# Optimization experiments

Hardware: AMD Instinct MI355X
Metric: run time of the kernel (lower is better)

Reference implementation:

```python
import jax, jax.numpy as jnp
import numpy as np
from math import factorial, sqrt

# ---- e3nn-style real Wigner-3j (Clebsch-Gordan) construction ----
L1, L2, LOUT, LMID = 3, 3, 3, 4

def _cg_coef(j1, m1, j2, m2, j3, m3):
    if m1 + m2 != m3:
        return 0.0
    f = factorial
    vmin = max(0, j2 - j3 - m1, j1 - j3 + m2)
    vmax = min(j1 + j2 - j3, j1 - m1, j2 + m2)
    pref = sqrt((2 * j3 + 1) * f(j3 + j1 - j2) * f(j3 - j1 + j2) * f(j1 + j2 - j3) / f(j1 + j2 + j3 + 1))
    pref *= sqrt(f(j3 + m3) * f(j3 - m3) * f(j1 + m1) * f(j1 - m1) * f(j2 + m2) * f(j2 - m2))
    s = 0.0
    for v in range(vmin, vmax + 1):
        s += (-1) ** v / (f(v) * f(j1 + j2 - j3 - v) * f(j1 - m1 - v) * f(j2 + m2 - v)
                          * f(j3 - j2 + m1 + v) * f(j3 - j1 - m2 + v))
    return pref * s

def _su2_cg(l1, l2, l3):
    C = np.zeros((2 * l1 + 1, 2 * l2 + 1, 2 * l3 + 1))
    for m1 in range(-l1, l1 + 1):
        for m2 in range(-l2, l2 + 1):
            m3 = m1 + m2
            if -l3 <= m3 <= l3:
                C[l1 + m1, l2 + m2, l3 + m3] = _cg_coef(l1, m1, l2, m2, l3, m3)
    return C

def _q(l):  # real->complex SH change of basis (e3nn convention)
    q = np.zeros((2 * l + 1, 2 * l + 1), dtype=np.complex128)
    for m in range(-l, 0):
        q[l + m, l + abs(m)] = 1 / np.sqrt(2)
        q[l + m, l - abs(m)] = -1j / np.sqrt(2)
    q[l, l] = 1.0
    for m in range(1, l + 1):
        q[l + m, l + abs(m)] = (-1) ** m / np.sqrt(2)
        q[l + m, l - abs(m)] = 1j * (-1) ** m / np.sqrt(2)
    return (-1j) ** l * q

def _w3j(l1, l2, l3):
    C = _su2_cg(l1, l2, l3).astype(np.complex128)
    C = np.einsum('ij,kl,mn,ikn->jlm', _q(l1), _q(l2), np.conj(_q(l3).T), C)
    C = np.real(C)
    return (C / np.linalg.norm(C)).astype(np.float32)

def _instructions(lmax1, lmax2, lmax_out):
    ins = [(a, b, c)
           for a in range(lmax1 + 1) for b in range(lmax2 + 1) for c in range(lmax_out + 1)
           if abs(a - b) <= c <= a + b and (a + b + c) % 2 == 0]
    cnt = {}
    for _, _, c in ins:
        cnt[c] = cnt.get(c, 0) + 1
    # normalization='component', path_normalization='element' with all mul=1
    pw = np.array([sqrt((2 * c + 1) / cnt[c]) for _, _, c in ins], dtype=np.float32)
    return ins, pw

INS1, PW1 = _instructions(L1, L2, LMID)      # 27 paths
INS21, PW21 = _instructions(L1, LMID, LOUT)  # 27 paths
INS22, PW22 = _instructions(L2, LMID, LOUT)  # 27 paths
W3J = {k: jnp.asarray(_w3j(*k)) for k in set(INS1) | set(INS21) | set(INS22)}

def _tp(x, y, w, ins, pw, lmax_out):
    # FullyConnectedTensorProduct with multiplicity-1 SH irreps.
    # x: [E, (l1+1)^2], y: [E, (l2+1)^2] -> [E, (lmax_out+1)^2]
    out = jnp.zeros((x.shape[0], (lmax_out + 1) ** 2), dtype=x.dtype)
    for i, (a, b, c) in enumerate(ins):
        xa = x[:, a * a:(a + 1) ** 2]
        yb = y[:, b * b:(b + 1) ** 2]
        z = jnp.einsum('ijk,ei,ej->ek', W3J[(a, b, c)], xa, yb)
        out = out.at[:, c * c:(c + 1) ** 2].add((pw[i] * w[i]) * z)
    return out

E, C = 200000, 16
B = (LOUT + 1) ** 2  # 16

def setup_inputs() -> dict:
    k = jax.random.split(jax.random.key(0), 5)
    return {
        'x': jax.random.normal(k[0], (E, B, C), jnp.float32),
        'y': jax.random.normal(k[1], (E, B, C), jnp.float32),
        'w1': jax.random.normal(k[2], (len(INS1),), jnp.float32),
        'w21': jax.random.normal(k[3], (len(INS21),), jnp.float32),
        'w22': jax.random.normal(k[4], (len(INS22),), jnp.float32),
    }

def reference(x, y, w1, w21, w22):
    xm = x.mean(2)  # [E, 16]
    ym = y.mean(2)  # [E, 16]
    mid = _tp(xm, ym, w1, INS1, PW1, LMID)  # [E, 25]
    out = (x + y
           + _tp(xm, mid, w21, INS21, PW21, LOUT)[..., None]
           + _tp(ym, mid, w22, INS22, PW22, LOUT)[..., None])
    return out
```

## Files before the change

### kernel.cpp

```cpp
#include <hip/hip_runtime.h>


struct W3JT { double v[9][9][9]; };

constexpr double dfact(int n) { double r = 1.0; for (int i = 2; i <= n; ++i) r *= (double)i; return r; }

constexpr double csqrt(double x) {
  if (x <= 0.0) return 0.0;
  double g = x > 1.0 ? x : 1.0;
  for (int i = 0; i < 80; ++i) g = 0.5 * (g + x / g);
  return g;
}

constexpr double cg_coef(int j1, int m1, int j2, int m2, int j3, int m3) {
  if (m1 + m2 != m3) return 0.0;
  int vmin = 0;
  if (j2 - j3 - m1 > vmin) vmin = j2 - j3 - m1;
  if (j1 - j3 + m2 > vmin) vmin = j1 - j3 + m2;
  int vmax = j1 + j2 - j3;
  if (j1 - m1 < vmax) vmax = j1 - m1;
  if (j2 + m2 < vmax) vmax = j2 + m2;
  double pref = csqrt((2.0 * j3 + 1.0) * dfact(j3 + j1 - j2) * dfact(j3 - j1 + j2) * dfact(j1 + j2 - j3) / dfact(j1 + j2 + j3 + 1));
  pref *= csqrt(dfact(j3 + m3) * dfact(j3 - m3) * dfact(j1 + m1) * dfact(j1 - m1) * dfact(j2 + m2) * dfact(j2 - m2));
  double s = 0.0;
  for (int v = vmin; v <= vmax; ++v) {
    double t = 1.0 / (dfact(v) * dfact(j1 + j2 - j3 - v) * dfact(j1 - m1 - v) * dfact(j2 + m2 - v) * dfact(j3 - j2 + m1 + v) * dfact(j3 - j1 - m2 + v));
    s += (v & 1) ? -t : t;
  }
  return pref * s;
}

struct QCol { int n; int row[2]; double re[2]; double im[2]; };

constexpr QCol qcol(int l, int col) {
  QCol q{};
  const int lm = l & 3;
  const double pr = (lm == 0) ? 1.0 : (lm == 2) ? -1.0 : 0.0;
  const double pi = (lm == 1) ? -1.0 : (lm == 3) ? 1.0 : 0.0;
  const int mu = col - l;
  const int am = mu < 0 ? -mu : mu;
  const double is2 = 0.70710678118654752440;
  if (mu == 0) {
    q.n = 1; q.row[0] = l;
    q.re[0] = pr; q.im[0] = pi;
  } else {
    const double s = (am & 1) ? -1.0 : 1.0;
    double a0 = 0.0, b0 = 0.0, a1 = 0.0, b1 = 0.0;
    if (mu > 0) { a0 = is2; b0 = 0.0;  a1 = s * is2; b1 = 0.0; }
    else        { a0 = 0.0; b0 = -is2; a1 = 0.0;     b1 = s * is2; }
    q.n = 2;
    q.row[0] = l - am; q.row[1] = l + am;
    q.re[0] = a0 * pr - b0 * pi; q.im[0] = a0 * pi + b0 * pr;
    q.re[1] = a1 * pr - b1 * pi; q.im[1] = a1 * pi + b1 * pr;
  }
  return q;
}

constexpr W3JT make_w3j(int l1, int l2, int l3) {
  W3JT R{};
  double C[9][9][9]{};
  for (int m1 = -l1; m1 <= l1; ++m1)
    for (int m2 = -l2; m2 <= l2; ++m2) {
      int m3 = m1 + m2;
      if (m3 >= -l3 && m3 <= l3)
        C[l1 + m1][l2 + m2][l3 + m3] = cg_coef(l1, m1, l2, m2, l3, m3);
    }
  double nrm = 0.0;
  for (int j = 0; j < 2 * l1 + 1; ++j) {
    QCol q1 = qcol(l1, j);
    for (int l = 0; l < 2 * l2 + 1; ++l) {
      QCol q2 = qcol(l2, l);
      for (int m = 0; m < 2 * l3 + 1; ++m) {
        QCol q3 = qcol(l3, m);
        double re = 0.0;
        for (int a = 0; a < q1.n; ++a)
          for (int b = 0; b < q2.n; ++b)
            for (int c = 0; c < q3.n; ++c) {
              double cv = C[q1.row[a]][q2.row[b]][q3.row[c]];
              if (cv == 0.0) continue;
              double ar = q1.re[a], ai = q1.im[a];
              double br = q2.re[b], bi = q2.im[b];
              double cr = q3.re[c], ci = -q3.im[c];
              double abr = ar * br - ai * bi;
              double abi = ar * bi + ai * br;
              double prr = abr * cr - abi * ci;
              re += prr * cv;
            }
        R.v[j][l][m] = re;
        nrm += re * re;
      }
    }
  }
  double n = csqrt(nrm);
  if (n > 0.0)
    for (int j = 0; j < 2 * l1 + 1; ++j)
      for (int l = 0; l < 2 * l2 + 1; ++l)
        for (int m = 0; m < 2 * l3 + 1; ++m)
          R.v[j][l][m] /= n;
  return R;
}

constexpr int CNT1[5] = {4, 6, 7, 6, 4};
constexpr int CNT2[4] = {4, 7, 8, 8};

#define NZCHK(V) ((V) > 1e-12 || (V) < -1e-12)

#define TP_MID(IDX, A, B, C) do { \
  constexpr W3JT T = make_w3j(A, B, C); \
  constexpr double PW = csqrt((2.0 * (C) + 1.0) / (double)CNT1[(C)]); \
  const float wi = w1p[IDX]; \
  float u[2 * (A) + 1]; \
  _Pragma("unroll") for (int i = 0; i < 2 * (A) + 1; ++i) u[i] = wi * xm[(A) * (A) + i]; \
  _Pragma("unroll") for (int i = 0; i < 2 * (A) + 1; ++i) { \
    _Pragma("unroll") for (int j = 0; j < 2 * (B) + 1; ++j) { \
      const float p_ = u[i] * ym[(B) * (B) + j]; \
      _Pragma("unroll") for (int k = 0; k < 2 * (C) + 1; ++k) { \
        if (NZCHK(T.v[i][j][k])) \
          mid[(C) * (C) + k] = __builtin_fmaf((float)(T.v[i][j][k] * PW), p_, mid[(C) * (C) + k]); \
      } \
    } \
  } \
} while (0)

#define TP_OUT(IDX, A, B, C) do { \
  constexpr W3JT T = make_w3j(A, B, C); \
  constexpr double PW = csqrt((2.0 * (C) + 1.0) / (double)CNT2[(C)]); \
  const float wa = w21p[IDX]; \
  const float wb = w22p[IDX]; \
  float u[2 * (A) + 1]; \
  _Pragma("unroll") for (int i = 0; i < 2 * (A) + 1; ++i) \
    u[i] = wa * xm[(A) * (A) + i] + wb * ym[(A) * (A) + i]; \
  _Pragma("unroll") for (int i = 0; i < 2 * (A) + 1; ++i) { \
    _Pragma("unroll") for (int j = 0; j < 2 * (B) + 1; ++j) { \
      const float p_ = u[i] * mid[(B) * (B) + j]; \
      _Pragma("unroll") for (int k = 0; k < 2 * (C) + 1; ++k) { \
        if (NZCHK(T.v[i][j][k])) \
          tv[(C) * (C) + k] = __builtin_fmaf((float)(T.v[i][j][k] * PW), p_, tv[(C) * (C) + k]); \
      } \
    } \
  } \
} while (0)

__global__ __launch_bounds__(512) void cg2_v15(
    const float4* __restrict__ x4, const float4* __restrict__ y4,
    const float* __restrict__ w1p, const float* __restrict__ w21p,
    const float* __restrict__ w22p, float4* __restrict__ o4, int E)
{
  __shared__ float lmx[128 * 32];
  __shared__ float ltv[128 * 16];

  const int eL = threadIdx.x >> 2;
  const int g  = threadIdx.x & 3;
  const int e  = blockIdx.x * 128 + eL;
  const bool ok = (e < E);
  const int base = e * 64 + g;

  float4 s[16];
  float px[16], py[16];
  if (ok) {
#pragma unroll
    for (int k = 0; k < 16; ++k) {
      const float4 xv = x4[base + 4 * k];
      const float4 yv = y4[base + 4 * k];
      s[k].x = xv.x + yv.x; s[k].y = xv.y + yv.y;
      s[k].z = xv.z + yv.z; s[k].w = xv.w + yv.w;
      px[k] = (xv.x + xv.y) + (xv.z + xv.w);
      py[k] = (yv.x + yv.y) + (yv.z + yv.w);
    }
  } else {
#pragma unroll
    for (int k = 0; k < 16; ++k) { px[k] = 0.f; py[k] = 0.f; }
  }

#pragma unroll
  for (int k = 0; k < 16; ++k) {
    float rx = px[k] + __shfl_xor(px[k], 1);
    rx += __shfl_xor(rx, 2);
    float ry = py[k] + __shfl_xor(py[k], 1);
    ry += __shfl_xor(ry, 2);
    px[k] = rx * (1.0f / 16.0f);
    py[k] = ry * (1.0f / 16.0f);
  }

  if (ok) {
#pragma unroll
    for (int u = 0; u < 4; ++u) {
      const int j = 4 * g + u;
      lmx[eL * 32 + ((j + eL) & 31)]      = px[j];
      lmx[eL * 32 + ((16 + j + eL) & 31)] = py[j];
    }
  }
  __syncthreads();

  if (threadIdx.x < 128) {
    const int q = threadIdx.x;
    const bool ok2 = (blockIdx.x * 128 + q < E);
    float xm[16], ym[16];
#pragma unroll
    for (int j = 0; j < 16; ++j) xm[j] = lmx[q * 32 + ((j + q) & 31)];
#pragma unroll
    for (int j = 0; j < 16; ++j) ym[j] = lmx[q * 32 + ((16 + j + q) & 31)];

    float mid[25];
#pragma unroll
    for (int k = 0; k < 25; ++k) mid[k] = 0.f;

    TP_MID( 0, 0, 0, 0);
    TP_MID( 1, 0, 1, 1);
    TP_MID( 2, 0, 2, 2);
    TP_MID( 3, 0, 3, 3);
    TP_MID( 4, 1, 0, 1);
    TP_MID( 5, 1, 1, 0);
    TP_MID( 6, 1, 1, 2);
    TP_MID( 7, 1, 2, 1);
    TP_MID( 8, 1, 2, 3);
    TP_MID( 9, 1, 3, 2);
    TP_MID(10, 1, 3, 4);
    TP_MID(11, 2, 0, 2);
    TP_MID(12, 2, 1, 1);
    TP_MID(13, 2, 1, 3);
    TP_MID(14, 2, 2, 0);
    TP_MID(15, 2, 2, 2);
    TP_MID(16, 2, 2, 4);
    TP_MID(17, 2, 3, 1);
    TP_MID(18, 2, 3, 3);
    TP_MID(19, 3, 0, 3);
    TP_MID(20, 3, 1, 2);
    TP_MID(21, 3, 1, 4);
    TP_MID(22, 3, 2, 1);
    TP_MID(23, 3, 2, 3);
    TP_MID(24, 3, 3, 0);
    TP_MID(25, 3, 3, 2);
    TP_MID(26, 3, 3, 4);

    float tv[16];
#pragma unroll
    for (int k = 0; k < 16; ++k) tv[k] = 0.f;

    TP_OUT( 0, 0, 0, 0);
    TP_OUT( 1, 0, 1, 1);
    TP_OUT( 2, 0, 2, 2);
    TP_OUT( 3, 0, 3, 3);
    TP_OUT( 4, 1, 0, 1);
    TP_OUT( 5, 1, 1, 0);
    TP_OUT( 6, 1, 1, 2);
    TP_OUT( 7, 1, 2, 1);
    TP_OUT( 8, 1, 2, 3);
    TP_OUT( 9, 1, 3, 2);
    TP_OUT(10, 1, 4, 3);
    TP_OUT(11, 2, 0, 2);
    TP_OUT(12, 2, 1, 1);
    TP_OUT(13, 2, 1, 3);
    TP_OUT(14, 2, 2, 0);
    TP_OUT(15, 2, 2, 2);
    TP_OUT(16, 2, 3, 1);
    TP_OUT(17, 2, 3, 3);
    TP_OUT(18, 2, 4, 2);
    TP_OUT(19, 3, 0, 3);
    TP_OUT(20, 3, 1, 2);
    TP_OUT(21, 3, 2, 1);
    TP_OUT(22, 3, 2, 3);
    TP_OUT(23, 3, 3, 0);
    TP_OUT(24, 3, 3, 2);
    TP_OUT(25, 3, 4, 1);
    TP_OUT(26, 3, 4, 3);

    if (ok2) {
#pragma unroll
      for (int k = 0; k < 16; ++k) ltv[q * 16 + ((k + q) & 15)] = tv[k];
    }
  }
  __syncthreads();

  if (ok) {
#pragma unroll
    for (int k = 0; k < 16; ++k) {
      const float t = ltv[eL * 16 + ((k + eL) & 15)];
      float4 o;
      o.x = s[k].x + t;
      o.y = s[k].y + t;
      o.z = s[k].z + t;
      o.w = s[k].w + t;
      o4[base + 4 * k] = o;
    }
  }
}

extern "C" void kernel_launch(void* const* d_in, const int* in_sizes, int n_in,
                              void* d_out, int out_size, void* d_ws, size_t ws_size,
                              hipStream_t stream) {
  const float4* x4 = (const float4*)d_in[0];
  const float4* y4 = (const float4*)d_in[1];
  const float* w1p = (const float*)d_in[2];
  const float* w21p = (const float*)d_in[3];
  const float* w22p = (const float*)d_in[4];
  float4* o4 = (float4*)d_out;

  const int E = in_sizes[0] / 256;
  const int block = 512;
  const int grid = (E + 127) / 128;

  cg2_v15<<<grid, block, 0, stream>>>(x4, y4, w1p, w21p, w22p, o4, E);
}
```

Baseline: 145.2 us.

## Process two edges per thread, store residual as bf16, group paths by output

Halves the block to 256 threads, with each thread loading two edges' x and y. The x+y residual is kept in registers as packed bf16 to cut register pressure. The tensor-product stages accumulate per output degree and read means and mid values from shared memory instead of holding large register arrays. The aim is to reduce register use and raise occupancy and memory parallelism, at the cost of bf16 rounding error in the residual term.

New measurement: 203.9 us. 1.4x slower.

```diff
diff --git a/kernel.cpp b/kernel.cpp
--- a/kernel.cpp
+++ b/kernel.cpp
@@ -105,183 +105,181 @@
 
 #define NZCHK(V) ((V) > 1e-12 || (V) < -1e-12)
 
-#define TP_MID(IDX, A, B, C) do { \
+#define LXM(J) lmx[q * 32 + (((J) + q) & 31)]
+#define LYM(J) lmx[q * 32 + ((16 + (J) + q) & 31)]
+
+#define TPM(IDX, A, B, C, ACC) do { \
   constexpr W3JT T = make_w3j(A, B, C); \
   constexpr double PW = csqrt((2.0 * (C) + 1.0) / (double)CNT1[(C)]); \
   const float wi = w1p[IDX]; \
-  float u[2 * (A) + 1]; \
-  _Pragma("unroll") for (int i = 0; i < 2 * (A) + 1; ++i) u[i] = wi * xm[(A) * (A) + i]; \
+  float u_[2 * (A) + 1], yv_[2 * (B) + 1]; \
+  _Pragma("unroll") for (int i = 0; i < 2 * (A) + 1; ++i) u_[i] = wi * LXM((A) * (A) + i); \
+  _Pragma("unroll") for (int j = 0; j < 2 * (B) + 1; ++j) yv_[j] = LYM((B) * (B) + j); \
   _Pragma("unroll") for (int i = 0; i < 2 * (A) + 1; ++i) { \
     _Pragma("unroll") for (int j = 0; j < 2 * (B) + 1; ++j) { \
-      const float p_ = u[i] * ym[(B) * (B) + j]; \
+      const float p_ = u_[i] * yv_[j]; \
       _Pragma("unroll") for (int k = 0; k < 2 * (C) + 1; ++k) { \
         if (NZCHK(T.v[i][j][k])) \
-          mid[(C) * (C) + k] = __builtin_fmaf((float)(T.v[i][j][k] * PW), p_, mid[(C) * (C) + k]); \
+          ACC[k] = __builtin_fmaf((float)(T.v[i][j][k] * PW), p_, ACC[k]); \
       } \
     } \
   } \
 } while (0)
 
-#define TP_OUT(IDX, A, B, C) do { \
+#define TPO(IDX, A, B, C, ACC) do { \
   constexpr W3JT T = make_w3j(A, B, C); \
   constexpr double PW = csqrt((2.0 * (C) + 1.0) / (double)CNT2[(C)]); \
   const float wa = w21p[IDX]; \
   const float wb = w22p[IDX]; \
-  float u[2 * (A) + 1]; \
+  float u_[2 * (A) + 1], mv_[2 * (B) + 1]; \
   _Pragma("unroll") for (int i = 0; i < 2 * (A) + 1; ++i) \
-    u[i] = wa * xm[(A) * (A) + i] + wb * ym[(A) * (A) + i]; \
+    u_[i] = wa * LXM((A) * (A) + i) + wb * LYM((A) * (A) + i); \
+  _Pragma("unroll") for (int j = 0; j < 2 * (B) + 1; ++j) mv_[j] = lmid[q * 27 + (B) * (B) + j]; \
   _Pragma("unroll") for (int i = 0; i < 2 * (A) + 1; ++i) { \
     _Pragma("unroll") for (int j = 0; j < 2 * (B) + 1; ++j) { \
-      const float p_ = u[i] * mid[(B) * (B) + j]; \
+      const float p_ = u_[i] * mv_[j]; \
       _Pragma("unroll") for (int k = 0; k < 2 * (C) + 1; ++k) { \
         if (NZCHK(T.v[i][j][k])) \
-          tv[(C) * (C) + k] = __builtin_fmaf((float)(T.v[i][j][k] * PW), p_, tv[(C) * (C) + k]); \
+          ACC[k] = __builtin_fmaf((float)(T.v[i][j][k] * PW), p_, ACC[k]); \
       } \
     } \
   } \
 } while (0)
 
-__global__ __launch_bounds__(512) void cg2_v15(
+__device__ __forceinline__ unsigned int bfr(float f) {
+  unsigned int u = __builtin_bit_cast(unsigned int, f);
+  return (u + 0x7fffu + ((u >> 16) & 1u)) >> 16;
+}
+__device__ __forceinline__ unsigned int pkbf(float a, float b) {
+  return bfr(a) | (bfr(b) << 16);
+}
+__device__ __forceinline__ float ubl(unsigned int u) { return __builtin_bit_cast(float, u << 16); }
+__device__ __forceinline__ float ubh(unsigned int u) { return __builtin_bit_cast(float, u & 0xffff0000u); }
+
+__global__ __launch_bounds__(256) void cg2_v18(
     const float4* __restrict__ x4, const float4* __restrict__ y4,
     const float* __restrict__ w1p, const float* __restrict__ w21p,
     const float* __restrict__ w22p, float4* __restrict__ o4, int E)
 {
   __shared__ float lmx[128 * 32];
+  __shared__ float lmid[128 * 27];
   __shared__ float ltv[128 * 16];
 
   const int eL = threadIdx.x >> 2;
   const int g  = threadIdx.x & 3;
-  const int e  = blockIdx.x * 128 + eL;
-  const bool ok = (e < E);
-  const int base = e * 64 + g;
-
-  float4 s[16];
-  float px[16], py[16];
-  if (ok) {
-#pragma unroll
-    for (int k = 0; k < 16; ++k) {
-      const float4 xv = x4[base + 4 * k];
-      const float4 yv = y4[base + 4 * k];
-      s[k].x = xv.x + yv.x; s[k].y = xv.y + yv.y;
-      s[k].z = xv.z + yv.z; s[k].w = xv.w + yv.w;
-      px[k] = (xv.x + xv.y) + (xv.z + xv.w);
-      py[k] = (yv.x + yv.y) + (yv.z + yv.w);
-    }
-  } else {
-#pragma unroll
-    for (int k = 0; k < 16; ++k) { px[k] = 0.f; py[k] = 0.f; }
-  }
-
+  const int e0 = blockIdx.x * 128;
+  const int eA = e0 + eL;
+  const int eB = eA + 64;
+  const bool okA = (eA < E), okB = (eB < E);
+  const int baseA = eA * 64 + g;
+  const int baseB = eB * 64 + g;
+
+  unsigned int sA0[16], sA1[16], sB0[16], sB1[16];
 #pragma unroll
   for (int k = 0; k < 16; ++k) {
-    float rx = px[k] + __shfl_xor(px[k], 1);
-    rx += __shfl_xor(rx, 2);
-    float ry = py[k] + __shfl_xor(py[k], 1);
-    ry += __shfl_xor(ry, 2);
-    px[k] = rx * (1.0f / 16.0f);
-    py[k] = ry * (1.0f / 16.0f);
-  }
-
-  if (ok) {
-#pragma unroll
-    for (int u = 0; u < 4; ++u) {
-      const int j = 4 * g + u;
-      lmx[eL * 32 + ((j + eL) & 31)]      = px[j];
-      lmx[eL * 32 + ((16 + j + eL) & 31)] = py[j];
+    float pxa = 0.f, pya = 0.f, pxb = 0.f, pyb = 0.f;
+    if (okA) {
+      const float4 xv = x4[baseA + 4 * k];
+      const float4 yv = y4[baseA + 4 * k];
+      sA0[k] = pkbf(xv.x + yv.x, xv.y + yv.y);
+      sA1[k] = pkbf(xv.z + yv.z, xv.w + yv.w);
+      pxa = (xv.x + xv.y) + (xv.z + xv.w);
+      pya = (yv.x + yv.y) + (yv.z + yv.w);
+    }
+    if (okB) {
+      const float4 xv = x4[baseB + 4 * k];
+      const float4 yv = y4[baseB + 4 * k];
+      sB0[k] = pkbf(xv.x + yv.x, xv.y + yv.y);
+      sB1[k] = pkbf(xv.z + yv.z, xv.w + yv.w);
+      pxb = (xv.x + xv.y) + (xv.z + xv.w);
+      pyb = (yv.x + yv.y) + (yv.z + yv.w);
+    }
+    pxa += __shfl_xor(pxa, 1); pxa += __shfl_xor(pxa, 2);
+    pya += __shfl_xor(pya, 1); pya += __shfl_xor(pya, 2);
+    pxb += __shfl_xor(pxb, 1); pxb += __shfl_xor(pxb, 2);
+    pyb += __shfl_xor(pyb, 1); pyb += __shfl_xor(pyb, 2);
+    if (g == 0) {
+      const int sw  = (k + eL) & 31;
+      const int swy = (16 + k + eL) & 31;
+      if (okA) {
+        lmx[eL * 32 + sw]  = pxa * (1.0f / 16.0f);
+        lmx[eL * 32 + swy] = pya * (1.0f / 16.0f);
+      }
+      if (okB) {
+        lmx[(eL + 64) * 32 + sw]  = pxb * (1.0f / 16.0f);
+        lmx[(eL + 64) * 32 + swy] = pyb * (1.0f / 16.0f);
+      }
     }
   }
   __syncthreads();
 
   if (threadIdx.x < 128) {
     const int q = threadIdx.x;
-    const bool ok2 = (blockIdx.x * 128 + q < E);
-    float xm[16], ym[16];
-#pragma unroll
-    for (int j = 0; j < 16; ++j) xm[j] = lmx[q * 32 + ((j + q) & 31)];
-#pragma unroll
-    for (int j = 0; j < 16; ++j) ym[j] = lmx[q * 32 + ((16 + j + q) & 31)];
-
-    float mid[25];
-#pragma unroll
-    for (int k = 0; k < 25; ++k) mid[k] = 0.f;
-
-    TP_MID( 0, 0, 0, 0);
-    TP_MID( 1, 0, 1, 1);
-    TP_MID( 2, 0, 2, 2);
-    TP_MID( 3, 0, 3, 3);
-    TP_MID( 4, 1, 0, 1);
-    TP_MID( 5, 1, 1, 0);
-    TP_MID( 6, 1, 1, 2);
-    TP_MID( 7, 1, 2, 1);
-    TP_MID( 8, 1, 2, 3);
-    TP_MID( 9, 1, 3, 2);
-    TP_MID(10, 1, 3, 4);
-    TP_MID(11, 2, 0, 2);
-    TP_MID(12, 2, 1, 1);
-    TP_MID(13, 2, 1, 3);
-    TP_MID(14, 2, 2, 0);
-    TP_MID(15, 2, 2, 2);
-    TP_MID(16, 2, 2, 4);
-    TP_MID(17, 2, 3, 1);
-    TP_MID(18, 2, 3, 3);
-    TP_MID(19, 3, 0, 3);
-    TP_MID(20, 3, 1, 2);
-    TP_MID(21, 3, 1, 4);
-    TP_MID(22, 3, 2, 1);
-    TP_MID(23, 3, 2, 3);
-    TP_MID(24, 3, 3, 0);
-    TP_MID(25, 3, 3, 2);
-    TP_MID(26, 3, 3, 4);
-
-    float tv[16];
-#pragma unroll
-    for (int k = 0; k < 16; ++k) tv[k] = 0.f;
-
-    TP_OUT( 0, 0, 0, 0);
-    TP_OUT( 1, 0, 1, 1);
-    TP_OUT( 2, 0, 2, 2);
-    TP_OUT( 3, 0, 3, 3);
-    TP_OUT( 4, 1, 0, 1);
-    TP_OUT( 5, 1, 1, 0);
-    TP_OUT( 6, 1, 1, 2);
-    TP_OUT( 7, 1, 2, 1);
-    TP_OUT( 8, 1, 2, 3);
-    TP_OUT( 9, 1, 3, 2);
-    TP_OUT(10, 1, 4, 3);
-    TP_OUT(11, 2, 0, 2);
-    TP_OUT(12, 2, 1, 1);
-    TP_OUT(13, 2, 1, 3);
-    TP_OUT(14, 2, 2, 0);
-    TP_OUT(15, 2, 2, 2);
-    TP_OUT(16, 2, 3, 1);
-    TP_OUT(17, 2, 3, 3);
-    TP_OUT(18, 2, 4, 2);
-    TP_OUT(19, 3, 0, 3);
-    TP_OUT(20, 3, 1, 2);
-    TP_OUT(21, 3, 2, 1);
-    TP_OUT(22, 3, 2, 3);
-    TP_OUT(23, 3, 3, 0);
-    TP_OUT(24, 3, 3, 2);
-    TP_OUT(25, 3, 4, 1);
-    TP_OUT(26, 3, 4, 3);
-
-    if (ok2) {
-#pragma unroll
-      for (int k = 0; k < 16; ++k) ltv[q * 16 + ((k + q) & 15)] = tv[k];
+    const bool okq = (e0 + q) < E;
+    if (okq) {
+      { float m0[1] = {0.f};
+        TPM( 0,0,0,0,m0); TPM( 5,1,1,0,m0); TPM(14,2,2,0,m0); TPM(24,3,3,0,m0);
+        lmid[q * 27 + 0] = m0[0]; }
+      { float m1[3] = {0.f,0.f,0.f};
+        TPM( 1,0,1,1,m1); TPM( 4,1,0,1,m1); TPM( 7,1,2,1,m1);
+        TPM(12,2,1,1,m1); TPM(17,2,3,1,m1); TPM(22,3,2,1,m1);
+#pragma unroll
+        for (int i = 0; i < 3; ++i) lmid[q * 27 + 1 + i] = m1[i]; }
+      { float m2[5] = {0.f,0.f,0.f,0.f,0.f};
+        TPM( 2,0,2,2,m2); TPM( 6,1,1,2,m2); TPM( 9,1,3,2,m2); TPM(11,2,0,2,m2);
+        TPM(15,2,2,2,m2); TPM(20,3,1,2,m2); TPM(25,3,3,2,m2);
+#pragma unroll
+        for (int i = 0; i < 5; ++i) lmid[q * 27 + 4 + i] = m2[i]; }
+      { float m3[7] = {0.f,0.f,0.f,0.f,0.f,0.f,0.f};
+        TPM( 3,0,3,3,m3); TPM( 8,1,2,3,m3); TPM(13,2,1,3,m3);
+        TPM(18,2,3,3,m3); TPM(19,3,0,3,m3); TPM(23,3,2,3,m3);
+#pragma unroll
+        for (int i = 0; i < 7; ++i) lmid[q * 27 + 9 + i] = m3[i]; }
+      { float m4[9] = {0.f,0.f,0.f,0.f,0.f,0.f,0.f,0.f,0.f};
+        TPM(10,1,3,4,m4); TPM(16,2,2,4,m4); TPM(21,3,1,4,m4); TPM(26,3,3,4,m4);
+#pragma unroll
+        for (int i = 0; i < 9; ++i) lmid[q * 27 + 16 + i] = m4[i]; }
+
+      asm volatile("" ::: "memory");
+
+      { float t0[1] = {0.f};
+        TPO( 0,0,0,0,t0); TPO( 5,1,1,0,t0); TPO(14,2,2,0,t0); TPO(23,3,3,0,t0);
+        ltv[q * 16 + ((0 + q) & 15)] = t0[0]; }
+      { float t1[3] = {0.f,0.f,0.f};
+        TPO( 1,0,1,1,t1); TPO( 4,1,0,1,t1); TPO( 7,1,2,1,t1); TPO(12,2,1,1,t1);
+        TPO(16,2,3,1,t1); TPO(21,3,2,1,t1); TPO(25,3,4,1,t1);
+#pragma unroll
+        for (int i = 0; i < 3; ++i) ltv[q * 16 + ((1 + i + q) & 15)] = t1[i]; }
+      { float t2[5] = {0.f,0.f,0.f,0.f,0.f};
+        TPO( 2,0,2,2,t2); TPO( 6,1,1,2,t2); TPO( 9,1,3,2,t2); TPO(11,2,0,2,t2);
+        TPO(15,2,2,2,t2); TPO(18,2,4,2,t2); TPO(20,3,1,2,t2); TPO(24,3,3,2,t2);
+#pragma unroll
+        for (int i = 0; i < 5; ++i) ltv[q * 16 + ((4 + i + q) & 15)] = t2[i]; }
+      { float t3[7] = {0.f,0.f,0.f,0.f,0.f,0.f,0.f};
+        TPO( 3,0,3,3,t3); TPO( 8,1,2,3,t3); TPO(10,1,4,3,t3); TPO(13,2,1,3,t3);
+        TPO(17,2,3,3,t3); TPO(19,3,0,3,t3); TPO(22,3,2,3,t3); TPO(26,3,4,3,t3);
+#pragma unroll
+        for (int i = 0; i < 7; ++i) ltv[q * 16 + ((9 + i + q) & 15)] = t3[i]; }
     }
   }
   __syncthreads();
 
-  if (ok) {
-#pragma unroll
-    for (int k = 0; k < 16; ++k) {
-      const float t = ltv[eL * 16 + ((k + eL) & 15)];
+#pragma unroll
+  for (int k = 0; k < 16; ++k) {
+    const int sw = (k + eL) & 15;
+    if (okA) {
+      const float t = ltv[eL * 16 + sw];
       float4 o;
-      o.x = s[k].x + t;
-      o.y = s[k].y + t;
-      o.z = s[k].z + t;
-      o.w = s[k].w + t;
-      o4[base + 4 * k] = o;
+      o.x = ubl(sA0[k]) + t; o.y = ubh(sA0[k]) + t;
+      o.z = ubl(sA1[k]) + t; o.w = ubh(sA1[k]) + t;
+      o4[baseA + 4 * k] = o;
+    }
+    if (okB) {
+      const float t = ltv[(eL + 64) * 16 + sw];
+      float4 o;
+      o.x = ubl(sB0[k]) + t; o.y = ubh(sB0[k]) + t;
+      o.z = ubl(sB1[k]) + t; o.w = ubh(sB1[k]) + t;
+      o4[baseB + 4 * k] = o;
     }
   }
 }
@@ -297,8 +295,8 @@
   float4* o4 = (float4*)d_out;
 
   const int E = in_sizes[0] / 256;
-  const int block = 512;
+  const int block = 256;
   const int grid = (E + 127) / 128;
 
-  cg2_v15<<<grid, block, 0, stream>>>(x4, y4, w1p, w21p, w22p, o4, E);
-}
+  cg2_v18<<<grid, block, 0, stream>>>(x4, y4, w1p, w21p, w22p, o4, E);
+}
```
